# Kernel optimization log

Hardware: AMD Instinct MI355X
Metric: run time of the kernel (lower is better)

## Reference

```python
import jax, jax.numpy as jnp
import numpy as np

EPS = 1e-5

def conv_bn(x, w, bn):
    # 1x1 conv (no bias) + BatchNorm2d in eval mode.
    # x: [B,C,H,W], w: [O,C], bn: [4,O] = (gamma, beta, running_mean, running_var)
    y = jnp.einsum('bchw,oc->bohw', x, w)
    g, b, m, v = bn[0], bn[1], bn[2], bn[3]
    s = g * jax.lax.rsqrt(v + EPS)
    return y * s[None, :, None, None] + (b - m * s)[None, :, None, None]

def setup_inputs() -> dict:
    key = jax.random.key(0)
    ks = jax.random.split(key, 10)
    dim, nh_kd, dh = 384, 256, 1024
    return {
        'x':   jax.random.normal(ks[0], (16, dim, 32, 32), dtype=jnp.float32),
        'wq':  jax.random.normal(ks[1], (nh_kd, dim), dtype=jnp.float32) * 0.05,
        'bnq': jax.random.uniform(ks[2], (4, nh_kd), dtype=jnp.float32),
        'wk':  jax.random.normal(ks[3], (nh_kd, dim), dtype=jnp.float32) * 0.05,
        'bnk': jax.random.uniform(ks[4], (4, nh_kd), dtype=jnp.float32),
        'wv':  jax.random.normal(ks[5], (dh, dim), dtype=jnp.float32) * 0.05,
        'bnv': jax.random.uniform(ks[6], (4, dh), dtype=jnp.float32),
        'wp':  jax.random.normal(ks[7], (dim, dh), dtype=jnp.float32) * 0.05,
        'bnp': jax.random.uniform(ks[8], (4, dim), dtype=jnp.float32),
        'num_heads': 8,
    }

def reference(x, wq, bnq, wk, bnk, wv, bnv, wp, bnp, num_heads):
    B, C, H, W = x.shape
    N = H * W
    nh = num_heads
    kd = wq.shape[0] // nh          # key_dim
    d = wv.shape[0] // nh           # attn_ratio * key_dim
    dh = wv.shape[0]
    scale = kd ** (-0.5)

    qq = conv_bn(x, wq, bnq).reshape(B, nh, kd, N).transpose(0, 1, 3, 2)  # [B,nh,N,kd]
    kk = conv_bn(x, wk, bnk).reshape(B, nh, kd, N)                         # [B,nh,kd,N]
    vv = conv_bn(x, wv, bnv).reshape(B, nh, d, N).transpose(0, 1, 3, 2)    # [B,nh,N,d]

    # NOTE: original divides by scale (i.e. multiplies by sqrt(key_dim)); kept faithfully.
    attn = jnp.einsum('bhnk,bhkm->bhnm', qq, kk) / scale
    attn = jax.nn.softmax(attn, axis=-1)
    xx = jnp.einsum('bhnm,bhmd->bhnd', attn, vv)           # [B,nh,N,d]
    xx = xx.transpose(0, 1, 3, 2).reshape(B, dh, H, W)
    return conv_bn(xx, wp, bnp)
```

## Files before the change

### kernel.cpp

```cpp
#include <hip/hip_runtime.h>

typedef _Float16 f16x8 __attribute__((ext_vector_type(8)));
typedef _Float16 f16x4 __attribute__((ext_vector_type(4)));
typedef __fp16 h16x2 __attribute__((ext_vector_type(2)));
typedef float f32x4 __attribute__((ext_vector_type(4)));
typedef float f32x16 __attribute__((ext_vector_type(16)));

#define BN_EPS 1e-5f
#define SQRT32 5.656854249492381f
#define LOG2E  1.4426950408889634f

typedef const __attribute__((address_space(1))) void* gas_p;
typedef __attribute__((address_space(3))) void* las_p;

__global__ __launch_bounds__(256) void prep(
    const float* __restrict__ x,
    const float* __restrict__ wq, const float* __restrict__ wk,
    const float* __restrict__ wv, const float* __restrict__ wp,
    const float* __restrict__ bnq, const float* __restrict__ bnk,
    const float* __restrict__ bnv, const float* __restrict__ bnp,
    _Float16* __restrict__ xT_hi, _Float16* __restrict__ xT_lo,
    _Float16* __restrict__ wqk_h, _Float16* __restrict__ wqk_l,
    _Float16* __restrict__ wv_h,  _Float16* __restrict__ wp_h,
    float* __restrict__ s_qkv, float* __restrict__ t_qkv,
    float* __restrict__ s_p,   float* __restrict__ t_p)
{
    __shared__ float Tx[64][65];
    const int t = threadIdx.x;
    if (blockIdx.z < 16) {
        const int ct = blockIdx.x, nt = blockIdx.y, b = blockIdx.z;
        const int c0 = ct * 64, n0 = nt * 64;
        {
            int tr = t >> 4, tc = (t & 15) * 4;
            #pragma unroll
            for (int p = 0; p < 4; p++) {
                int r = tr + p * 16;
                float4 v = *(const float4*)(x + ((size_t)(b * 384 + c0 + r)) * 1024 + n0 + tc);
                Tx[r][tc + 0] = v.x; Tx[r][tc + 1] = v.y; Tx[r][tc + 2] = v.z; Tx[r][tc + 3] = v.w;
            }
        }
        __syncthreads();
        {
            int nn = t >> 2, cc = (t & 3) * 16;
            f16x8 h0, h1, l0, l1;
            #pragma unroll
            for (int i = 0; i < 8; i++) {
                float v = Tx[cc + i][nn];
                _Float16 hh = (_Float16)v;
                h0[i] = hh; l0[i] = (_Float16)(v - (float)hh);
            }
            #pragma unroll
            for (int i = 0; i < 8; i++) {
                float v = Tx[cc + 8 + i][nn];
                _Float16 hh = (_Float16)v;
                h1[i] = hh; l1[i] = (_Float16)(v - (float)hh);
            }
            size_t o = ((size_t)(b * 1024 + n0 + nn)) * 384 + c0 + cc;
            *(f16x8*)(xT_hi + o) = h0; *(f16x8*)(xT_hi + o + 8) = h1;
            *(f16x8*)(xT_lo + o) = l0; *(f16x8*)(xT_lo + o + 8) = l1;
        }
    } else {
        const int NQK = 512 * 384, NV = 1024 * 384, NP = 384 * 1024;
        int tid = (blockIdx.y * 6 + blockIdx.x) * 256 + t;
        for (int i = tid; i < NQK + NV + NP; i += 24576) {
            if (i < NQK) {
                int o = i / 384, c = i - o * 384;
                float v = (o < 256) ? wq[o * 384 + c] : wk[(o - 256) * 384 + c];
                _Float16 hh = (_Float16)v;
                wqk_h[i] = hh; wqk_l[i] = (_Float16)(v - (float)hh);
            } else if (i < NQK + NV) {
                wv_h[i - NQK] = (_Float16)wv[i - NQK];
            } else {
                wp_h[i - NQK - NV] = (_Float16)wp[i - NQK - NV];
            }
        }
        if (tid < 1536) {
            int i = tid;
            float g, be, m, v;
            if (i < 256)      { int o = i;       g = bnq[o]; be = bnq[256 + o];  m = bnq[512 + o];  v = bnq[768 + o]; }
            else if (i < 512) { int o = i - 256; g = bnk[o]; be = bnk[256 + o];  m = bnk[512 + o];  v = bnk[768 + o]; }
            else              { int o = i - 512; g = bnv[o]; be = bnv[1024 + o]; m = bnv[2048 + o]; v = bnv[3072 + o]; }
            float s = g * rsqrtf(v + BN_EPS);
            float tt = be - m * s;
            if (i < 256) { s *= SQRT32 * LOG2E; tt *= SQRT32 * LOG2E; }
            s_qkv[i] = s; t_qkv[i] = tt;
        } else if (tid < 1536 + 384) {
            int o = tid - 1536;
            float g = bnp[o], be = bnp[384 + o], m = bnp[768 + o], v = bnp[1152 + o];
            float s = g * rsqrtf(v + BN_EPS);
            s_p[o] = s; t_p[o] = be - m * s;
        }
    }
}

__global__ __launch_bounds__(256, 2) void gemm_qkv(
    const _Float16* __restrict__ wqk_h, const _Float16* __restrict__ wqk_l,
    const _Float16* __restrict__ wv_h,
    const _Float16* __restrict__ xT_hi, const _Float16* __restrict__ xT_lo,
    const float* __restrict__ S, const float* __restrict__ T,
    _Float16* __restrict__ qT_h, _Float16* __restrict__ qT_l,
    _Float16* __restrict__ kT_h, _Float16* __restrict__ kT_l,
    _Float16* __restrict__ vbuf)
{
    __shared__ __align__(16) _Float16 As_h[128 * 40];
    __shared__ __align__(16) _Float16 As_l[128 * 40];
    __shared__ __align__(16) _Float16 Bs_h[128 * 40];
    __shared__ __align__(16) _Float16 Bs_l[128 * 40];
    const int t = threadIdx.x, lane = t & 63, w = t >> 6;
    const int wr = w >> 1, wc = w & 1, l16 = lane & 15, lq = lane >> 4;
    const int bx = blockIdx.x, n0 = blockIdx.y * 128, b = blockIdx.z;
    const bool isv = bx >= 4;
    const int o0 = isv ? (bx - 4) * 128 : bx * 128;
    const _Float16* __restrict__ Ah = isv ? wv_h : wqk_h;

    f32x4 acc[4][4] = {};

    for (int kb = 0; kb < 384; kb += 32) {
        __syncthreads();
        #pragma unroll
        for (int p = 0; p < 2; p++) {
            int g = t + p * 256, row = g >> 2, ch = g & 3;
            *(uint4*)(&As_h[row * 40 + ch * 8]) =
                *(const uint4*)(Ah + (size_t)(o0 + row) * 384 + kb + ch * 8);
        }
        #pragma unroll
        for (int p = 0; p < 2; p++) {
            int g = t + p * 256, row = g >> 2, ch = g & 3;
            *(uint4*)(&Bs_h[row * 40 + ch * 8]) =
                *(const uint4*)(xT_hi + ((size_t)(b * 1024) + n0 + row) * 384 + kb + ch * 8);
        }
        if (!isv) {
            #pragma unroll
            for (int p = 0; p < 2; p++) {
                int g = t + p * 256, row = g >> 2, ch = g & 3;
                *(uint4*)(&As_l[row * 40 + ch * 8]) =
                    *(const uint4*)(wqk_l + (size_t)(o0 + row) * 384 + kb + ch * 8);
            }
            #pragma unroll
            for (int p = 0; p < 2; p++) {
                int g = t + p * 256, row = g >> 2, ch = g & 3;
                *(uint4*)(&Bs_l[row * 40 + ch * 8]) =
                    *(const uint4*)(xT_lo + ((size_t)(b * 1024) + n0 + row) * 384 + kb + ch * 8);
            }
        }
        __syncthreads();

        if (!isv) {
            f16x8 ah[4], al[4], bh[4], bl[4];
            #pragma unroll
            for (int i = 0; i < 4; i++) {
                ah[i] = *(const f16x8*)(&Bs_h[(wr * 64 + i * 16 + l16) * 40 + lq * 8]);
                al[i] = *(const f16x8*)(&Bs_l[(wr * 64 + i * 16 + l16) * 40 + lq * 8]);
            }
            #pragma unroll
            for (int j = 0; j < 4; j++) {
                bh[j] = *(const f16x8*)(&As_h[(wc * 64 + j * 16 + l16) * 40 + lq * 8]);
                bl[j] = *(const f16x8*)(&As_l[(wc * 64 + j * 16 + l16) * 40 + lq * 8]);
            }
            #pragma unroll
            for (int i = 0; i < 4; i++)
                #pragma unroll
                for (int j = 0; j < 4; j++) {
                    acc[i][j] = __builtin_amdgcn_mfma_f32_16x16x32_f16(ah[i], bh[j], acc[i][j], 0, 0, 0);
                    acc[i][j] = __builtin_amdgcn_mfma_f32_16x16x32_f16(al[i], bh[j], acc[i][j], 0, 0, 0);
                    acc[i][j] = __builtin_amdgcn_mfma_f32_16x16x32_f16(ah[i], bl[j], acc[i][j], 0, 0, 0);
                }
        } else {
            f16x8 a[4], bf[4];
            #pragma unroll
            for (int i = 0; i < 4; i++) a[i]  = *(const f16x8*)(&As_h[(wr * 64 + i * 16 + l16) * 40 + lq * 8]);
            #pragma unroll
            for (int j = 0; j < 4; j++) bf[j] = *(const f16x8*)(&Bs_h[(wc * 64 + j * 16 + l16) * 40 + lq * 8]);
            #pragma unroll
            for (int i = 0; i < 4; i++)
                #pragma unroll
                for (int j = 0; j < 4; j++)
                    acc[i][j] = __builtin_amdgcn_mfma_f32_16x16x32_f16(a[i], bf[j], acc[i][j], 0, 0, 0);
        }
    }

    if (!isv) {
        #pragma unroll
        for (int i = 0; i < 4; i++) {
            #pragma unroll
            for (int r = 0; r < 4; r++) {
                int n = n0 + wr * 64 + i * 16 + lq * 4 + r;
                #pragma unroll
                for (int j = 0; j < 4; j++) {
                    int o = o0 + wc * 64 + j * 16 + l16;
                    float sc = S[o], sh = T[o];
                    float v = acc[i][j][r] * sc + sh;
                    _Float16 hh = (_Float16)v;
                    _Float16 ll = (_Float16)(v - (float)hh);
                    if (o < 256) {
                        size_t idx = (((size_t)(b * 8) + (o >> 5)) * 1024 + n) * 32 + (o & 31);
                        qT_h[idx] = hh; qT_l[idx] = ll;
                    } else {
                        int oo = o - 256;
                        int hd = oo >> 5, c = oo & 31;
                        int f = ((n >> 5) & 1) * 2 + (c >> 4);
                        size_t idx = ((((size_t)(b * 8 + hd) * 16 + (n >> 6)) * 4 + f) * 64
                                      + ((c >> 3) & 1) * 32 + (n & 31)) * 8 + (c & 7);
                        kT_h[idx] = hh; kT_l[idx] = ll;
                    }
                }
            }
        }
    } else {
        #pragma unroll
        for (int i = 0; i < 4; i++) {
            #pragma unroll
            for (int r = 0; r < 4; r++) {
                int o = o0 + wr * 64 + i * 16 + lq * 4 + r;
                float sc = S[512 + o], sh = T[512 + o];
                #pragma unroll
                for (int j = 0; j < 4; j++) {
                    int n = n0 + wc * 64 + j * 16 + l16;
                    int k = n & 63;
                    int s4 = k >> 4, c4 = (k >> 2) & 3;
                    int ep = s4 * 16 + (c4 & 1) * 8 + (c4 >> 1) * 4 + (k & 3);
                    int nst = (n & ~63) | ep;
                    vbuf[((size_t)(b * 1024) + o) * 1024 + nst] = (_Float16)(acc[i][j][r] * sc + sh);
                }
            }
        }
    }
}

__device__ __forceinline__ f32x16 qk6(f16x8 kh0, f16x8 kl0, f16x8 kh1, f16x8 kl1,
                                      f16x8 qh0, f16x8 ql0, f16x8 qh1, f16x8 ql1) {
    f32x16 c = {};
    c = __builtin_amdgcn_mfma_f32_32x32x16_f16(kh0, qh0, c, 0, 0, 0);
    c = __builtin_amdgcn_mfma_f32_32x32x16_f16(kl0, qh0, c, 0, 0, 0);
    c = __builtin_amdgcn_mfma_f32_32x32x16_f16(kh0, ql0, c, 0, 0, 0);
    c = __builtin_amdgcn_mfma_f32_32x32x16_f16(kh1, qh1, c, 0, 0, 0);
    c = __builtin_amdgcn_mfma_f32_32x32x16_f16(kl1, qh1, c, 0, 0, 0);
    c = __builtin_amdgcn_mfma_f32_32x32x16_f16(kh1, ql1, c, 0, 0, 0);
    return c;
}

__global__ __launch_bounds__(256, 2) void attn(
    const _Float16* __restrict__ qT_h, const _Float16* __restrict__ qT_l,
    const _Float16* __restrict__ kT_h, const _Float16* __restrict__ kT_l,
    const _Float16* __restrict__ vbuf,
    _Float16* __restrict__ xxT_h, _Float16* __restrict__ xxT_l)
{
    __shared__ __align__(16) _Float16 Vs[3][128 * 64];
    __shared__ __align__(16) _Float16 Ksh[2][2048];
    __shared__ __align__(16) _Float16 Ksl[2][2048];
    const int t = threadIdx.x, lane = t & 63, w = t >> 6;
    const int L = lane & 31, hl = lane >> 5;
    const int bh = blockIdx.x, qt = blockIdx.y;
    const int b = bh >> 3, h = bh & 7;
    const size_t vbase = ((size_t)(b * 1024) + h * 128) * 1024;

    f16x8 bq_h[2], bq_l[2];
    {
        int q = qt * 128 + w * 32 + L;
        #pragma unroll
        for (int kh = 0; kh < 2; kh++) {
            size_t base = ((size_t)(bh * 1024) + q) * 32 + kh * 16 + hl * 8;
            bq_h[kh] = *(const f16x8*)(qT_h + base);
            bq_l[kh] = *(const f16x8*)(qT_l + base);
        }
    }

    f32x16 o_acc[4] = {};
    float m_st = -INFINITY, l_st = 0.f;
    f16x8 pf[4];

    #define DMA_TILE(vb, kb, kt_)                                                  \
        {                                                                          \
            size_t ktb = (size_t)(bh * 16 + (kt_)) * 2048 + (size_t)t * 8;         \
            __builtin_amdgcn_global_load_lds((gas_p)(const void*)(kT_h + ktb),     \
                                             (las_p)(void*)&Ksh[kb][w * 512], 16, 0, 0); \
            __builtin_amdgcn_global_load_lds((gas_p)(const void*)(kT_l + ktb),     \
                                             (las_p)(void*)&Ksl[kb][w * 512], 16, 0, 0); \
            _Pragma("unroll")                                                      \
            for (int p = 0; p < 4; p++) {                                          \
                int g2 = t + p * 256;                                              \
                int d = g2 >> 3;                                                   \
                int kcg = (g2 & 7) ^ (d & 7);                                      \
                const _Float16* src = vbuf + vbase + (size_t)d * 1024              \
                                      + (kt_) * 64 + kcg * 8;                      \
                _Float16* dst = &Vs[vb][(p * 256 + w * 64) * 8];                   \
                __builtin_amdgcn_global_load_lds((gas_p)(const void*)src,          \
                                                 (las_p)(void*)dst, 16, 0, 0);     \
            }                                                                      \
        }

    DMA_TILE(0, 0, 0)
    __syncthreads();

    for (int kt = 0; kt < 16; kt++) {
        const int kcur = kt & 1;
        const int vprv = (kt + 2) % 3;

        if (kt < 15) DMA_TILE((kt + 1) % 3, kcur ^ 1, kt + 1)

        const _Float16* khp = &Ksh[kcur][lane * 8];
        const _Float16* klp = &Ksl[kcur][lane * 8];
        f16x8 K0h = *(const f16x8*)(khp);
        f16x8 K1h = *(const f16x8*)(khp + 512);
        f16x8 K2h = *(const f16x8*)(khp + 1024);
        f16x8 K3h = *(const f16x8*)(khp + 1536);
        f16x8 K0l = *(const f16x8*)(klp);
        f16x8 K1l = *(const f16x8*)(klp + 512);
        f16x8 K2l = *(const f16x8*)(klp + 1024);
        f16x8 K3l = *(const f16x8*)(klp + 1536);

        __builtin_amdgcn_s_setprio(1);
        f32x16 c0 = qk6(K0h, K0l, K1h, K1l, bq_h[0], bq_l[0], bq_h[1], bq_l[1]);
        f32x16 c1 = qk6(K2h, K2l, K3h, K3l, bq_h[0], bq_l[0], bq_h[1], bq_l[1]);
        __builtin_amdgcn_s_setprio(0);

        if (kt) {
            __builtin_amdgcn_s_setprio(1);
            #pragma unroll
            for (int s = 0; s < 4; s++) {
                int cp = (2 * s + hl) ^ (L & 7);
                #pragma unroll
                for (int dt = 0; dt < 4; dt++) {
                    f16x8 avp = *(const f16x8*)(&Vs[vprv][(dt * 32 + L) * 64 + cp * 8]);
                    o_acc[dt] = __builtin_amdgcn_mfma_f32_32x32x16_f16(avp, pf[s], o_acc[dt], 0, 0, 0);
                }
            }
            __builtin_amdgcn_s_setprio(0);
        }

        #define EL(e) ((e) < 16 ? c0[e] : c1[(e) - 16])
        float t1[11];
        #pragma unroll
        for (int g = 0; g < 10; g++)
            t1[g] = fmaxf(fmaxf(EL(3 * g), EL(3 * g + 1)), EL(3 * g + 2));
        t1[10] = fmaxf(EL(30), EL(31));
        #undef EL
        float t2a = fmaxf(fmaxf(t1[0], t1[1]), t1[2]);
        float t2b = fmaxf(fmaxf(t1[3], t1[4]), t1[5]);
        float t2c = fmaxf(fmaxf(t1[6], t1[7]), t1[8]);
        float t2d = fmaxf(t1[9], t1[10]);
        float mx0 = fmaxf(fmaxf(t2a, t2b), fmaxf(t2c, t2d));
        float mx = fmaxf(mx0, __shfl_xor(mx0, 32, 64));

        if (__any(mx > m_st + 8.f)) {
            float mnew = fmaxf(m_st, mx);
            float a = exp2f(m_st - mnew);
            l_st *= a;
            #pragma unroll
            for (int dt = 0; dt < 4; dt++)
                #pragma unroll
                for (int i = 0; i < 16; i++) o_acc[dt][i] *= a;
            m_st = mnew;
        }

        float rs = 0.f;
        #pragma unroll
        for (int s = 0; s < 4; s++) {
            float pv[8];
            #pragma unroll
            for (int j = 0; j < 8; j++) {
                float cv = (s < 2) ? c0[(s & 1) * 8 + j] : c1[(s & 1) * 8 + j];
                pv[j] = exp2f(cv - m_st);
            }
            rs += ((pv[0] + pv[1]) + (pv[2] + pv[3])) + ((pv[4] + pv[5]) + (pv[6] + pv[7]));
            union { f16x8 v; h16x2 hh[4]; } u;
            #pragma unroll
            for (int j = 0; j < 4; j++)
                u.hh[j] = __builtin_amdgcn_cvt_pkrtz(pv[2 * j], pv[2 * j + 1]);
            pf[s] = u.v;
        }
        l_st += rs;

        if (kt < 15) __syncthreads();
    }
    #undef DMA_TILE

    {
        __builtin_amdgcn_s_setprio(1);
        #pragma unroll
        for (int s = 0; s < 4; s++) {
            int cp = (2 * s + hl) ^ (L & 7);
            #pragma unroll
            for (int dt = 0; dt < 4; dt++) {
                f16x8 avp = *(const f16x8*)(&Vs[0][(dt * 32 + L) * 64 + cp * 8]);
                o_acc[dt] = __builtin_amdgcn_mfma_f32_32x32x16_f16(avp, pf[s], o_acc[dt], 0, 0, 0);
            }
        }
        __builtin_amdgcn_s_setprio(0);
    }

    l_st += __shfl_xor(l_st, 32, 64);

    {
        float rl = 1.f / l_st;
        int q = qt * 128 + w * 32 + L;
        #pragma unroll
        for (int dt = 0; dt < 4; dt++) {
            #pragma unroll
            for (int gg = 0; gg < 4; gg++) {
                f16x4 hv, lv;
                #pragma unroll
                for (int rr = 0; rr < 4; rr++) {
                    float v = o_acc[dt][gg * 4 + rr] * rl;
                    _Float16 hh = (_Float16)v;
                    hv[rr] = hh; lv[rr] = (_Float16)(v - (float)hh);
                }
                size_t o = ((size_t)(b * 1024) + q) * 1024 + h * 128 + dt * 32 + gg * 8 + hl * 4;
                *(f16x4*)(xxT_h + o) = hv;
                *(f16x4*)(xxT_l + o) = lv;
            }
        }
    }
}

__global__ __launch_bounds__(256, 2) void gemm_out(
    const _Float16* __restrict__ wp_h,
    const _Float16* __restrict__ xxT_h, const _Float16* __restrict__ xxT_l,
    const float* __restrict__ S, const float* __restrict__ T,
    float* __restrict__ out)
{
    __shared__ __align__(16) _Float16 As[128 * 40];
    __shared__ __align__(16) _Float16 Bh[64 * 40];
    __shared__ __align__(16) _Float16 Bl[64 * 40];
    const int t = threadIdx.x, lane = t & 63, w = t >> 6;
    const int wr = w >> 1, wc = w & 1, l16 = lane & 15, lq = lane >> 4;
    const int o0 = blockIdx.x * 128, n0 = blockIdx.y * 64, b = blockIdx.z;

    f32x4 acc[4][2] = {};

    for (int kb = 0; kb < 1024; kb += 32) {
        __syncthreads();
        #pragma unroll
        for (int p = 0; p < 2; p++) {
            int g = t + p * 256, row = g >> 2, ch = g & 3;
            *(uint4*)(&As[row * 40 + ch * 8]) =
                *(const uint4*)(wp_h + (size_t)(o0 + row) * 1024 + kb + ch * 8);
        }
        {
            int row = t >> 2, ch = t & 3;
            size_t src = ((size_t)(b * 1024) + n0 + row) * 1024 + kb + ch * 8;
            *(uint4*)(&Bh[row * 40 + ch * 8]) = *(const uint4*)(xxT_h + src);
            *(uint4*)(&Bl[row * 40 + ch * 8]) = *(const uint4*)(xxT_l + src);
        }
        __syncthreads();

        f16x8 a[4], bh[2], bl[2];
        #pragma unroll
        for (int i = 0; i < 4; i++) a[i] = *(const f16x8*)(&As[(wr * 64 + i * 16 + l16) * 40 + lq * 8]);
        #pragma unroll
        for (int j = 0; j < 2; j++) {
            bh[j] = *(const f16x8*)(&Bh[(wc * 32 + j * 16 + l16) * 40 + lq * 8]);
            bl[j] = *(const f16x8*)(&Bl[(wc * 32 + j * 16 + l16) * 40 + lq * 8]);
        }
        #pragma unroll
        for (int i = 0; i < 4; i++)
            #pragma unroll
            for (int j = 0; j < 2; j++) {
                acc[i][j] = __builtin_amdgcn_mfma_f32_16x16x32_f16(a[i], bh[j], acc[i][j], 0, 0, 0);
                acc[i][j] = __builtin_amdgcn_mfma_f32_16x16x32_f16(a[i], bl[j], acc[i][j], 0, 0, 0);
            }
    }

    #pragma unroll
    for (int i = 0; i < 4; i++) {
        #pragma unroll
        for (int r = 0; r < 4; r++) {
            int o = o0 + wr * 64 + i * 16 + lq * 4 + r;
            float sc = S[o], sh = T[o];
            #pragma unroll
            for (int j = 0; j < 2; j++) {
                int n = n0 + wc * 32 + j * 16 + l16;
                out[((size_t)(b * 384) + o) * 1024 + n] = acc[i][j][r] * sc + sh;
            }
        }
    }
}


extern "C" void kernel_launch(void* const* d_in, const int* in_sizes, int n_in,
                              void* d_out, int out_size, void* d_ws, size_t ws_size,
                              hipStream_t stream) {
    const float* x   = (const float*)d_in[0];
    const float* wq  = (const float*)d_in[1];
    const float* bnq = (const float*)d_in[2];
    const float* wk  = (const float*)d_in[3];
    const float* bnk = (const float*)d_in[4];
    const float* wv  = (const float*)d_in[5];
    const float* bnv = (const float*)d_in[6];
    const float* wp  = (const float*)d_in[7];
    const float* bnp = (const float*)d_in[8];
    float* out = (float*)d_out;
    (void)in_sizes; (void)n_in; (void)out_size; (void)ws_size;

    char* ws = (char*)d_ws;
    size_t off = 0;
    auto alloc = [&](size_t bytes) {
        void* p = ws + off;
        off = (off + bytes + 255) & ~(size_t)255;
        return p;
    };
    _Float16* xT_hi = (_Float16*)alloc((size_t)16 * 1024 * 384 * 2);
    _Float16* xT_lo = (_Float16*)alloc((size_t)16 * 1024 * 384 * 2);
    _Float16* wqk_h = (_Float16*)alloc((size_t)512 * 384 * 2);
    _Float16* wqk_l = (_Float16*)alloc((size_t)512 * 384 * 2);
    _Float16* wv_h  = (_Float16*)alloc((size_t)1024 * 384 * 2);
    alloc((size_t)7 * 1024 * 1024);
    _Float16* xxT_h = (_Float16*)d_ws;
    _Float16* wp_h  = (_Float16*)alloc((size_t)384 * 1024 * 2);
    float*    s_qkv = (float*)alloc(1536 * 4);
    float*    t_qkv = (float*)alloc(1536 * 4);
    float*    s_p   = (float*)alloc(384 * 4);
    float*    t_p   = (float*)alloc(384 * 4);
    _Float16* qT_h  = (_Float16*)alloc((size_t)16 * 8 * 1024 * 32 * 2);
    _Float16* qT_l  = (_Float16*)alloc((size_t)16 * 8 * 1024 * 32 * 2);
    _Float16* kT_h  = (_Float16*)alloc((size_t)16 * 8 * 1024 * 32 * 2);
    _Float16* kT_l  = (_Float16*)alloc((size_t)16 * 8 * 1024 * 32 * 2);
    _Float16* vbuf  = (_Float16*)alloc((size_t)16 * 1024 * 1024 * 2);
    _Float16* xxT_l = (_Float16*)alloc((size_t)16 * 1024 * 1024 * 2);

    prep<<<dim3(6, 16, 17), dim3(256), 0, stream>>>(
        x, wq, wk, wv, wp, bnq, bnk, bnv, bnp,
        xT_hi, xT_lo, wqk_h, wqk_l, wv_h, wp_h, s_qkv, t_qkv, s_p, t_p);

    gemm_qkv<<<dim3(12, 8, 16), dim3(256), 0, stream>>>(
        wqk_h, wqk_l, wv_h, xT_hi, xT_lo, s_qkv, t_qkv,
        qT_h, qT_l, kT_h, kT_l, vbuf);

    attn<<<dim3(128, 8), dim3(256), 0, stream>>>(qT_h, qT_l, kT_h, kT_l, vbuf, xxT_h, xxT_l);

    gemm_out<<<dim3(3, 16, 16), dim3(256), 0, stream>>>(wp_h, xxT_h, xxT_l, s_p, t_p, out);
}
```

Measured before the change: 307.2 us.

## Use direct global-to-LDS loads with XOR-swizzled 64-wide K tiles in GEMMs

Both projection GEMMs (QKV and output) now stage tiles with global_load_lds, which copies global memory straight into shared memory without passing through registers. The K-tile doubles from 32 to 64. A padded row stride is replaced by an XOR swizzle on 16-byte chunks to avoid LDS bank conflicts. This halves the number of barrier pairs per K-loop and frees registers, at the cost of twice the shared memory per block, which may limit occupancy.

```diff
diff --git a/kernel.cpp b/kernel.cpp
--- a/kernel.cpp
+++ b/kernel.cpp
@@ -102,10 +102,10 @@
     _Float16* __restrict__ kT_h, _Float16* __restrict__ kT_l,
     _Float16* __restrict__ vbuf)
 {
-    __shared__ __align__(16) _Float16 As_h[128 * 40];
-    __shared__ __align__(16) _Float16 As_l[128 * 40];
-    __shared__ __align__(16) _Float16 Bs_h[128 * 40];
-    __shared__ __align__(16) _Float16 Bs_l[128 * 40];
+    __shared__ __align__(16) _Float16 As_h[128 * 64];
+    __shared__ __align__(16) _Float16 As_l[128 * 64];
+    __shared__ __align__(16) _Float16 Bs_h[128 * 64];
+    __shared__ __align__(16) _Float16 Bs_l[128 * 64];
     const int t = threadIdx.x, lane = t & 63, w = t >> 6;
     const int wr = w >> 1, wc = w & 1, l16 = lane & 15, lq = lane >> 4;
     const int bx = blockIdx.x, n0 = blockIdx.y * 128, b = blockIdx.z;
@@ -115,67 +115,87 @@
 
     f32x4 acc[4][4] = {};
 
-    for (int kb = 0; kb < 384; kb += 32) {
+    for (int kb = 0; kb < 384; kb += 64) {
         __syncthreads();
         #pragma unroll
-        for (int p = 0; p < 2; p++) {
-            int g = t + p * 256, row = g >> 2, ch = g & 3;
-            *(uint4*)(&As_h[row * 40 + ch * 8]) =
-                *(const uint4*)(Ah + (size_t)(o0 + row) * 384 + kb + ch * 8);
-        }
-        #pragma unroll
-        for (int p = 0; p < 2; p++) {
-            int g = t + p * 256, row = g >> 2, ch = g & 3;
-            *(uint4*)(&Bs_h[row * 40 + ch * 8]) =
-                *(const uint4*)(xT_hi + ((size_t)(b * 1024) + n0 + row) * 384 + kb + ch * 8);
+        for (int p = 0; p < 4; p++) {
+            int g = t + p * 256, row = g >> 3, s = g & 7;
+            int col = ((s ^ (row & 7)) * 8);
+            __builtin_amdgcn_global_load_lds(
+                (gas_p)(const void*)(Ah + (size_t)(o0 + row) * 384 + kb + col),
+                (las_p)(void*)&As_h[(p * 256 + w * 64) * 8], 16, 0, 0);
+        }
+        #pragma unroll
+        for (int p = 0; p < 4; p++) {
+            int g = t + p * 256, row = g >> 3, s = g & 7;
+            int col = ((s ^ (row & 7)) * 8);
+            __builtin_amdgcn_global_load_lds(
+                (gas_p)(const void*)(xT_hi + ((size_t)(b * 1024) + n0 + row) * 384 + kb + col),
+                (las_p)(void*)&Bs_h[(p * 256 + w * 64) * 8], 16, 0, 0);
         }
         if (!isv) {
             #pragma unroll
-            for (int p = 0; p < 2; p++) {
-                int g = t + p * 256, row = g >> 2, ch = g & 3;
-                *(uint4*)(&As_l[row * 40 + ch * 8]) =
-                    *(const uint4*)(wqk_l + (size_t)(o0 + row) * 384 + kb + ch * 8);
-            }
-            #pragma unroll
-            for (int p = 0; p < 2; p++) {
-                int g = t + p * 256, row = g >> 2, ch = g & 3;
-                *(uint4*)(&Bs_l[row * 40 + ch * 8]) =
-                    *(const uint4*)(xT_lo + ((size_t)(b * 1024) + n0 + row) * 384 + kb + ch * 8);
+            for (int p = 0; p < 4; p++) {
+                int g = t + p * 256, row = g >> 3, s = g & 7;
+                int col = ((s ^ (row & 7)) * 8);
+                __builtin_amdgcn_global_load_lds(
+                    (gas_p)(const void*)(wqk_l + (size_t)(o0 + row) * 384 + kb + col),
+                    (las_p)(void*)&As_l[(p * 256 + w * 64) * 8], 16, 0, 0);
+            }
+            #pragma unroll
+            for (int p = 0; p < 4; p++) {
+                int g = t + p * 256, row = g >> 3, s = g & 7;
+                int col = ((s ^ (row & 7)) * 8);
+                __builtin_amdgcn_global_load_lds(
+                    (gas_p)(const void*)(xT_lo + ((size_t)(b * 1024) + n0 + row) * 384 + kb + col),
+                    (las_p)(void*)&Bs_l[(p * 256 + w * 64) * 8], 16, 0, 0);
             }
         }
         __syncthreads();
 
         if (!isv) {
-            f16x8 ah[4], al[4], bh[4], bl[4];
-            #pragma unroll
-            for (int i = 0; i < 4; i++) {
-                ah[i] = *(const f16x8*)(&Bs_h[(wr * 64 + i * 16 + l16) * 40 + lq * 8]);
-                al[i] = *(const f16x8*)(&Bs_l[(wr * 64 + i * 16 + l16) * 40 + lq * 8]);
-            }
-            #pragma unroll
-            for (int j = 0; j < 4; j++) {
-                bh[j] = *(const f16x8*)(&As_h[(wc * 64 + j * 16 + l16) * 40 + lq * 8]);
-                bl[j] = *(const f16x8*)(&As_l[(wc * 64 + j * 16 + l16) * 40 + lq * 8]);
-            }
-            #pragma unroll
-            for (int i = 0; i < 4; i++)
+            #pragma unroll
+            for (int kk = 0; kk < 2; kk++) {
+                const int sl = ((kk * 4 + lq) ^ (l16 & 7)) * 8;
+                f16x8 ah[4], al[4], bh[4], bl[4];
+                #pragma unroll
+                for (int i = 0; i < 4; i++) {
+                    int row = wr * 64 + i * 16 + l16;
+                    ah[i] = *(const f16x8*)(&Bs_h[row * 64 + sl]);
+                    al[i] = *(const f16x8*)(&Bs_l[row * 64 + sl]);
+                }
                 #pragma unroll
                 for (int j = 0; j < 4; j++) {
-                    acc[i][j] = __builtin_amdgcn_mfma_f32_16x16x32_f16(ah[i], bh[j], acc[i][j], 0, 0, 0);
-                    acc[i][j] = __builtin_amdgcn_mfma_f32_16x16x32_f16(al[i], bh[j], acc[i][j], 0, 0, 0);
-                    acc[i][j] = __builtin_amdgcn_mfma_f32_16x16x32_f16(ah[i], bl[j], acc[i][j], 0, 0, 0);
-                }
+                    int row = wc * 64 + j * 16 + l16;
+                    bh[j] = *(const f16x8*)(&As_h[row * 64 + sl]);
+                    bl[j] = *(const f16x8*)(&As_l[row * 64 + sl]);
+                }
+                #pragma unroll
+                for (int i = 0; i < 4; i++)
+                    #pragma unroll
+                    for (int j = 0; j < 4; j++) {
+                        acc[i][j] = __builtin_amdgcn_mfma_f32_16x16x32_f16(ah[i], bh[j], acc[i][j], 0, 0, 0);
+                        acc[i][j] = __builtin_amdgcn_mfma_f32_16x16x32_f16(al[i], bh[j], acc[i][j], 0, 0, 0);
+                        acc[i][j] = __builtin_amdgcn_mfma_f32_16x16x32_f16(ah[i], bl[j], acc[i][j], 0, 0, 0);
+                    }
+            }
         } else {
-            f16x8 a[4], bf[4];
-            #pragma unroll
-            for (int i = 0; i < 4; i++) a[i]  = *(const f16x8*)(&As_h[(wr * 64 + i * 16 + l16) * 40 + lq * 8]);
-            #pragma unroll
-            for (int j = 0; j < 4; j++) bf[j] = *(const f16x8*)(&Bs_h[(wc * 64 + j * 16 + l16) * 40 + lq * 8]);
-            #pragma unroll
-            for (int i = 0; i < 4; i++)
+            #pragma unroll
+            for (int kk = 0; kk < 2; kk++) {
+                const int sl = ((kk * 4 + lq) ^ (l16 & 7)) * 8;
+                f16x8 a[4], bf[4];
+                #pragma unroll
+                for (int i = 0; i < 4; i++)
+                    a[i] = *(const f16x8*)(&As_h[(wr * 64 + i * 16 + l16) * 64 + sl]);
                 #pragma unroll
                 for (int j = 0; j < 4; j++)
-                    acc[i][j] = __builtin_amdgcn_mfma_f32_16x16x32_f16(a[i], bf[j], acc[i][j], 0, 0, 0);
+                    bf[j] = *(const f16x8*)(&Bs_h[(wc * 64 + j * 16 + l16) * 64 + sl]);
+                #pragma unroll
+                for (int i = 0; i < 4; i++)
+                    #pragma unroll
+                    for (int j = 0; j < 4; j++)
+                        acc[i][j] = __builtin_amdgcn_mfma_f32_16x16x32_f16(a[i], bf[j], acc[i][j], 0, 0, 0);
+            }
         }
     }
 
@@ -419,46 +439,60 @@
     const float* __restrict__ S, const float* __restrict__ T,
     float* __restrict__ out)
 {
-    __shared__ __align__(16) _Float16 As[128 * 40];
-    __shared__ __align__(16) _Float16 Bh[64 * 40];
-    __shared__ __align__(16) _Float16 Bl[64 * 40];
+    __shared__ __align__(16) _Float16 As[128 * 64];
+    __shared__ __align__(16) _Float16 Bh[64 * 64];
+    __shared__ __align__(16) _Float16 Bl[64 * 64];
     const int t = threadIdx.x, lane = t & 63, w = t >> 6;
     const int wr = w >> 1, wc = w & 1, l16 = lane & 15, lq = lane >> 4;
     const int o0 = blockIdx.x * 128, n0 = blockIdx.y * 64, b = blockIdx.z;
 
     f32x4 acc[4][2] = {};
 
-    for (int kb = 0; kb < 1024; kb += 32) {
+    for (int kb = 0; kb < 1024; kb += 64) {
         __syncthreads();
         #pragma unroll
+        for (int p = 0; p < 4; p++) {
+            int g = t + p * 256, row = g >> 3, s = g & 7;
+            int col = ((s ^ (row & 7)) * 8);
+            __builtin_amdgcn_global_load_lds(
+                (gas_p)(const void*)(wp_h + (size_t)(o0 + row) * 1024 + kb + col),
+                (las_p)(void*)&As[(p * 256 + w * 64) * 8], 16, 0, 0);
+        }
+        #pragma unroll
         for (int p = 0; p < 2; p++) {
-            int g = t + p * 256, row = g >> 2, ch = g & 3;
-            *(uint4*)(&As[row * 40 + ch * 8]) =
-                *(const uint4*)(wp_h + (size_t)(o0 + row) * 1024 + kb + ch * 8);
-        }
-        {
-            int row = t >> 2, ch = t & 3;
-            size_t src = ((size_t)(b * 1024) + n0 + row) * 1024 + kb + ch * 8;
-            *(uint4*)(&Bh[row * 40 + ch * 8]) = *(const uint4*)(xxT_h + src);
-            *(uint4*)(&Bl[row * 40 + ch * 8]) = *(const uint4*)(xxT_l + src);
+            int g = t + p * 256, row = g >> 3, s = g & 7;
+            int col = ((s ^ (row & 7)) * 8);
+            size_t src = ((size_t)(b * 1024) + n0 + row) * 1024 + kb + col;
+            __builtin_amdgcn_global_load_lds(
+                (gas_p)(const void*)(xxT_h + src),
+                (las_p)(void*)&Bh[(p * 256 + w * 64) * 8], 16, 0, 0);
+            __builtin_amdgcn_global_load_lds(
+                (gas_p)(const void*)(xxT_l + src),
+                (las_p)(void*)&Bl[(p * 256 + w * 64) * 8], 16, 0, 0);
         }
         __syncthreads();
 
-        f16x8 a[4], bh[2], bl[2];
-        #pragma unroll
-        for (int i = 0; i < 4; i++) a[i] = *(const f16x8*)(&As[(wr * 64 + i * 16 + l16) * 40 + lq * 8]);
-        #pragma unroll
-        for (int j = 0; j < 2; j++) {
-            bh[j] = *(const f16x8*)(&Bh[(wc * 32 + j * 16 + l16) * 40 + lq * 8]);
-            bl[j] = *(const f16x8*)(&Bl[(wc * 32 + j * 16 + l16) * 40 + lq * 8]);
-        }
-        #pragma unroll
-        for (int i = 0; i < 4; i++)
+        #pragma unroll
+        for (int kk = 0; kk < 2; kk++) {
+            const int sl = ((kk * 4 + lq) ^ (l16 & 7)) * 8;
+            f16x8 a[4], bh2[2], bl2[2];
+            #pragma unroll
+            for (int i = 0; i < 4; i++)
+                a[i] = *(const f16x8*)(&As[(wr * 64 + i * 16 + l16) * 64 + sl]);
             #pragma unroll
             for (int j = 0; j < 2; j++) {
-                acc[i][j] = __builtin_amdgcn_mfma_f32_16x16x32_f16(a[i], bh[j], acc[i][j], 0, 0, 0);
-                acc[i][j] = __builtin_amdgcn_mfma_f32_16x16x32_f16(a[i], bl[j], acc[i][j], 0, 0, 0);
-            }
+                int row = wc * 32 + j * 16 + l16;
+                bh2[j] = *(const f16x8*)(&Bh[row * 64 + sl]);
+                bl2[j] = *(const f16x8*)(&Bl[row * 64 + sl]);
+            }
+            #pragma unroll
+            for (int i = 0; i < 4; i++)
+                #pragma unroll
+                for (int j = 0; j < 2; j++) {
+                    acc[i][j] = __builtin_amdgcn_mfma_f32_16x16x32_f16(a[i], bh2[j], acc[i][j], 0, 0, 0);
+                    acc[i][j] = __builtin_amdgcn_mfma_f32_16x16x32_f16(a[i], bl2[j], acc[i][j], 0, 0, 0);
+                }
+        }
     }
 
     #pragma unroll
```

Result: faster. 283.7 us (-7.7%).
